# Optimization experiments

Measured on AMD Instinct MI355X. Metric: run time of the kernel, lower is better.

Reference implementation:

```python
import jax, jax.numpy as jnp
import numpy as np

D_MODEL = 2048
N_HEADS = 16
HEAD_DIM = D_MODEL // N_HEADS
SCALE = HEAD_DIM ** -0.5
LN_EPS = 1e-5
N_LAYERS = 24


def _layernorm(x, g, b):
    mu = jnp.mean(x, axis=-1, keepdims=True)
    var = jnp.mean(jnp.square(x - mu), axis=-1, keepdims=True)
    return (x - mu) * jax.lax.rsqrt(var + LN_EPS) * g + b


def _split_heads(x):  # [B,S,D] -> [B,H,S,hd]
    B, S, _ = x.shape
    return x.reshape(B, S, N_HEADS, HEAD_DIM).transpose(0, 2, 1, 3)


def setup_inputs() -> dict:
    key = jax.random.key(0)
    ks = jax.random.split(key, 12)
    B, St, Si = 2, 2048, 1024
    std_qkv = D_MODEL ** -0.5
    std_o = (2 * N_LAYERS) ** -0.5
    return {
        "q_text": jax.random.normal(ks[0], (B, St, D_MODEL), jnp.float32),
        "q_image": jax.random.normal(ks[1], (B, Si, D_MODEL), jnp.float32),
        "k_text": jax.random.normal(ks[2], (B, St, D_MODEL), jnp.float32),
        "k_image": jax.random.normal(ks[3], (B, Si, D_MODEL), jnp.float32),
        "Wq": jax.random.normal(ks[4], (D_MODEL, D_MODEL), jnp.float32) * std_qkv,
        "Wk": jax.random.normal(ks[5], (D_MODEL, D_MODEL), jnp.float32) * std_qkv,
        "Wv": jax.random.normal(ks[6], (D_MODEL, D_MODEL), jnp.float32) * std_qkv,
        "Wo": jax.random.normal(ks[7], (D_MODEL, D_MODEL), jnp.float32) * std_o,
        "ln_text_g": jnp.ones((D_MODEL,), jnp.float32),
        "ln_text_b": jnp.zeros((D_MODEL,), jnp.float32),
        "ln_image_g": jnp.ones((D_MODEL,), jnp.float32),
        "ln_image_b": jnp.zeros((D_MODEL,), jnp.float32),
    }


def reference(q_text, q_image, k_text, k_image, Wq, Wk, Wv, Wo,
              ln_text_g, ln_text_b, ln_image_g, ln_image_b):
    # Normalize each key modality once, project to K/V, concat along seq.
    kt = _layernorm(k_text, ln_text_g, ln_text_b)
    ki = _layernorm(k_image, ln_image_g, ln_image_b)
    concat_k = jnp.concatenate([_split_heads(kt @ Wk.T), _split_heads(ki @ Wk.T)], axis=2)
    concat_v = jnp.concatenate([_split_heads(kt @ Wv.T), _split_heads(ki @ Wv.T)], axis=2)

    def attend(q, g, b):
        B, S, _ = q.shape
        qn = _layernorm(q, g, b)
        qh = _split_heads(qn @ Wq.T) * SCALE            # [B,H,Sq,hd]
        scores = jnp.einsum('bhqd,bhkd->bhqk', qh, concat_k)
        attn = jax.nn.softmax(scores.astype(jnp.float32), axis=-1).astype(q.dtype)
        out = jnp.einsum('bhqk,bhkd->bhqd', attn, concat_v)
        out = out.transpose(0, 2, 1, 3).reshape(B, S, D_MODEL)
        return out @ Wo.T

    out_text = attend(q_text, ln_text_g, ln_text_b)
    out_image = attend(q_image, ln_image_g, ln_image_b)
    return (out_text, out_image)
```

## Files before the change

### kernel.cpp

```cpp
#include <hip/hip_runtime.h>

typedef __attribute__((ext_vector_type(8))) short bf16x8;
typedef __attribute__((ext_vector_type(4))) float f32x4;
typedef __attribute__((ext_vector_type(8))) unsigned short u16x8;

#define D_MODEL 2048
#define NH 16
#define HD 128
#define SKV 3072
#define QK_SCALE 0.08838834764831845f
#define LOG2E 1.4426950408889634f
#define DEFER_THR 11.5413f

__device__ __forceinline__ unsigned short f2bf(float f) {
  unsigned int u = __float_as_uint(f);
  u += 0x7fffu + ((u >> 16) & 1u);
  return (unsigned short)(u >> 16);
}
__device__ __forceinline__ float exp2hw(float x) {
  float r; asm("v_exp_f32 %0, %1" : "=v"(r) : "v"(x)); return r;
}
__device__ __forceinline__ unsigned int cvtpk(float lo, float hi) {
  unsigned int r; asm("v_cvt_pk_bf16_f32 %0, %1, %2" : "=v"(r) : "v"(lo), "v"(hi)); return r;
}

typedef __attribute__((address_space(1))) void as1_void;
typedef __attribute__((address_space(3))) void as3_void;
__device__ __forceinline__ void gload_lds16(const void* g, void* l) {
  __builtin_amdgcn_global_load_lds((as1_void*)g, (as3_void*)l, 16, 0, 0);
}

#define MFMA16(a, b, c) __builtin_amdgcn_mfma_f32_16x16x32_bf16((a), (b), (c), 0, 0, 0)

__global__ __launch_bounds__(256) void cvt_w_kernel(
    const float* __restrict__ s0, const float* __restrict__ s1,
    const float* __restrict__ s2, const float* __restrict__ s3,
    unsigned short* __restrict__ dstbase) {
  const int y = blockIdx.y;
  const float* src = (y == 0) ? s0 : (y == 1) ? s1 : (y == 2) ? s2 : s3;
  const float scale = (y == 0) ? (QK_SCALE * LOG2E) : 1.0f;
  unsigned short* dst = dstbase + (size_t)y * 4194304;
  int i = blockIdx.x * 256 + threadIdx.x;
  const float4* s = (const float4*)src + (size_t)i * 2;
  float4 a = s[0], b = s[1];
  u16x8 r;
  r[0] = f2bf(a.x * scale); r[1] = f2bf(a.y * scale);
  r[2] = f2bf(a.z * scale); r[3] = f2bf(a.w * scale);
  r[4] = f2bf(b.x * scale); r[5] = f2bf(b.y * scale);
  r[6] = f2bf(b.z * scale); r[7] = f2bf(b.w * scale);
  *((u16x8*)dst + i) = r;
}

__global__ __launch_bounds__(256) void ln_kernel(
    const float* __restrict__ x, const float* __restrict__ gw,
    const float* __restrict__ bw, unsigned short* __restrict__ out,
    int spb, int orpb, int obase) {
  const int row = blockIdx.x;
  const int t = threadIdx.x;
  const int b = row / spb, s = row - b * spb;
  const float* xr = x + (size_t)row * D_MODEL;
  unsigned short* orow = out + ((size_t)b * orpb + obase + s) * D_MODEL;

  float4 v0 = *(const float4*)(xr + t * 8);
  float4 v1 = *(const float4*)(xr + t * 8 + 4);
  float sum = v0.x + v0.y + v0.z + v0.w + v1.x + v1.y + v1.z + v1.w;
  float sq  = v0.x*v0.x + v0.y*v0.y + v0.z*v0.z + v0.w*v0.w
            + v1.x*v1.x + v1.y*v1.y + v1.z*v1.z + v1.w*v1.w;
#pragma unroll
  for (int o = 32; o > 0; o >>= 1) {
    sum += __shfl_down(sum, o);
    sq  += __shfl_down(sq, o);
  }
  __shared__ float red[8];
  const int wv = t >> 6, l = t & 63;
  if (l == 0) { red[wv] = sum; red[4 + wv] = sq; }
  __syncthreads();
  sum = red[0] + red[1] + red[2] + red[3];
  sq  = red[4] + red[5] + red[6] + red[7];
  const float mu = sum * (1.0f / 2048.0f);
  const float var = sq * (1.0f / 2048.0f) - mu * mu;
  const float rs = rsqrtf(var + 1e-5f);

  float4 g0 = *(const float4*)(gw + t * 8);
  float4 g1 = *(const float4*)(gw + t * 8 + 4);
  float4 b0 = *(const float4*)(bw + t * 8);
  float4 b1 = *(const float4*)(bw + t * 8 + 4);
  u16x8 r;
  r[0] = f2bf((v0.x - mu) * rs * g0.x + b0.x);
  r[1] = f2bf((v0.y - mu) * rs * g0.y + b0.y);
  r[2] = f2bf((v0.z - mu) * rs * g0.z + b0.z);
  r[3] = f2bf((v0.w - mu) * rs * g0.w + b0.w);
  r[4] = f2bf((v1.x - mu) * rs * g1.x + b1.x);
  r[5] = f2bf((v1.y - mu) * rs * g1.y + b1.y);
  r[6] = f2bf((v1.z - mu) * rs * g1.z + b1.z);
  r[7] = f2bf((v1.w - mu) * rs * g1.w + b1.w);
  *(u16x8*)(orow + t * 8) = r;
}

__global__ __launch_bounds__(256, 2) void gemm256x_kernel(
    const unsigned short* __restrict__ Aq, const unsigned short* __restrict__ Akv,
    const unsigned short* __restrict__ Wq, const unsigned short* __restrict__ Wk,
    const unsigned short* __restrict__ Wv,
    void* __restrict__ d0, void* __restrict__ d1,
    void* __restrict__ d2, void* __restrict__ d3, int mode) {
  __shared__ unsigned short lds3[3][12288];

  const int tid = threadIdx.x;
  const int wid = tid >> 6, l = tid & 63;
  const int wm = wid >> 1, wn = wid & 1;
  const int fr = l & 15, fg = l >> 4;
  const int rc = (fg * 8) ^ ((fr & 3) << 3);

  const int cpx = gridDim.x >> 3;
  int wg = ((int)blockIdx.x & 7) * cpx + ((int)blockIdx.x >> 3);

  const unsigned short* A = Aq;
  const unsigned short* W = Wq;
  int emode = mode;
  if (mode == 10) {
    int mat = wg / 384; wg -= mat * 384;
    if (mat == 0)      { emode = 0; }
    else if (mat == 1) { emode = 3; A = Akv; W = Wk; }
    else               { emode = 1; A = Akv; W = Wv; }
  }
  const int bm = wg >> 4, bn = wg & 15;

  const int lr = l >> 2;
  const int gsw = ((l & 3) ^ (lr & 3)) * 8;
  const unsigned short* gaBase = A + (size_t)(bm * 256 + wid * 64 + lr) * 2048 + gsw;
  const unsigned short* gbBase = W + (size_t)(bn * 128 + wid * 32 + lr) * 2048 + gsw;

#define STAGE(buf, kt) do {                                          \
    unsigned short* _da = &lds3[(buf)][wid * 2048];                  \
    unsigned short* _db = &lds3[(buf)][8192 + wid * 1024];           \
    const unsigned short* _sa = gaBase + (size_t)(kt) * 32;          \
    const unsigned short* _sb = gbBase + (size_t)(kt) * 32;          \
    gload_lds16(_sa,             _da);                               \
    gload_lds16(_sa + 16 * 2048, _da + 512);                         \
    gload_lds16(_sa + 32 * 2048, _da + 1024);                        \
    gload_lds16(_sa + 48 * 2048, _da + 1536);                        \
    gload_lds16(_sb,             _db);                               \
    gload_lds16(_sb + 16 * 2048, _db + 512);                         \
  } while (0)

  f32x4 acc[8][4] = {};
  bf16x8 af[8], bf01[2], bf23[2];

  STAGE(0, 0);
  STAGE(1, 1);
  asm volatile("s_waitcnt vmcnt(6)" ::: "memory");
  __builtin_amdgcn_s_barrier();
#pragma unroll
  for (int mi = 0; mi < 8; ++mi)
    af[mi] = *(const bf16x8*)&lds3[0][(wm * 128 + mi * 16 + fr) * 32 + rc];
#pragma unroll
  for (int ni = 0; ni < 2; ++ni)
    bf01[ni] = *(const bf16x8*)&lds3[0][8192 + (wn * 64 + ni * 16 + fr) * 32 + rc];

  int cur = 0;
  for (int t = 0; t < 64; ++t) {
#pragma unroll
    for (int ni = 0; ni < 2; ++ni)
      bf23[ni] = *(const bf16x8*)&lds3[cur][8192 + (wn * 64 + (ni + 2) * 16 + fr) * 32 + rc];
    if (t < 62) {
      int stg = cur + 2; if (stg >= 3) stg -= 3;
      STAGE(stg, t + 2);
    }

    __builtin_amdgcn_s_setprio(1);
#pragma unroll
    for (int mi = 0; mi < 8; ++mi)
#pragma unroll
      for (int ni = 0; ni < 2; ++ni)
        acc[mi][ni] = MFMA16(af[mi], bf01[ni], acc[mi][ni]);
    __builtin_amdgcn_s_setprio(0);

    __builtin_amdgcn_s_setprio(1);
#pragma unroll
    for (int mi = 0; mi < 8; ++mi)
#pragma unroll
      for (int ni = 0; ni < 2; ++ni)
        acc[mi][ni + 2] = MFMA16(af[mi], bf23[ni], acc[mi][ni + 2]);
    __builtin_amdgcn_s_setprio(0);

    __builtin_amdgcn_sched_barrier(0);
    if (t < 62) {
      asm volatile("s_waitcnt vmcnt(6)" ::: "memory");
      __builtin_amdgcn_s_barrier();
    } else if (t == 62) {
      asm volatile("s_waitcnt vmcnt(0)" ::: "memory");
      __builtin_amdgcn_s_barrier();
    }

    int nxt = cur + 1; if (nxt >= 3) nxt -= 3;
    if (t < 63) {
#pragma unroll
      for (int mi = 0; mi < 8; ++mi)
        af[mi] = *(const bf16x8*)&lds3[nxt][(wm * 128 + mi * 16 + fr) * 32 + rc];
#pragma unroll
      for (int ni = 0; ni < 2; ++ni)
        bf01[ni] = *(const bf16x8*)&lds3[nxt][8192 + (wn * 64 + ni * 16 + fr) * 32 + rc];
    }
    cur = nxt;
  }
#undef STAGE

#pragma unroll
  for (int mi = 0; mi < 8; ++mi) {
    const int row0 = bm * 256 + wm * 128 + mi * 16 + fg * 4;
    if (emode == 1) {
      int b = row0 / 3072, s0 = row0 - b * 3072;
#pragma unroll
      for (int ni = 0; ni < 4; ++ni) {
        int col = bn * 128 + wn * 64 + ni * 16 + fr;
        int hh = col >> 7, d = col & 127;
        size_t bh = (size_t)(b * NH + hh);
        size_t idx = (bh * 128 + d) * (size_t)3072 + ((s0 & ~31) | ((s0 & 31) ^ ((d & 3) << 3)));
        uint2 pk;
        pk.x = cvtpk(acc[mi][ni][0], acc[mi][ni][1]);
        pk.y = cvtpk(acc[mi][ni][2], acc[mi][ni][3]);
        *(uint2*)((unsigned short*)d3 + idx) = pk;
      }
    } else {
#pragma unroll
      for (int r = 0; r < 4; ++r) {
        int row = row0 + r;
#pragma unroll
        for (int ni = 0; ni < 4; ++ni) {
          int col = bn * 128 + wn * 64 + ni * 16 + fr;
          float v = acc[mi][ni][r];
          if (emode == 2) {
            ((float*)d0)[(size_t)row * 2048 + col] = v;
          } else if (emode == 0) {
            int hh = col >> 7, d = col & 127;
            if (row < 4096) {
              int b = row >> 11, s = row & 2047;
              ((unsigned short*)d0)[((size_t)(b * NH + hh) * 2048 + s) * 128 + d] = f2bf(v);
            } else {
              int rr = row - 4096, b = rr >> 10, s = rr & 1023;
              ((unsigned short*)d1)[((size_t)(b * NH + hh) * 1024 + s) * 128 + d] = f2bf(v);
            }
          } else {
            int b = row / 3072, s = row - b * 3072;
            int hh = col >> 7, d = col & 127;
            size_t bh = (size_t)(b * NH + hh);
            ((unsigned short*)d2)[(bh * 3072 + s) * 128 + (d ^ ((s & 7) << 3))] = f2bf(v);
          }
        }
      }
    }
  }
}

__global__ __launch_bounds__(256, 3) void attn_kernel(
    const unsigned short* __restrict__ Qt, const unsigned short* __restrict__ Qi,
    const unsigned short* __restrict__ Kh, const unsigned short* __restrict__ Vt,
    unsigned short* __restrict__ AOt, unsigned short* __restrict__ AOi) {
  __shared__ unsigned short Sh[20480];

  const int lin = blockIdx.x;
  const int w768 = (lin & 7) * 96 + (lin >> 3);
  const int qt24 = w768 % 24;
  const int hb   = w768 / 24;
  const int h = hb & 15, b = hb >> 4;
  const bool is_text = qt24 < 16;
  const int qt = is_text ? qt24 : qt24 - 16;
  const int Sq = is_text ? 2048 : 1024;
  const unsigned short* Qh = is_text ? Qt : Qi;
  unsigned short* AO = is_text ? AOt : AOi;

  const int tid = threadIdx.x;
  const int w = tid >> 6, l = tid & 63;
  const int fr = l & 15, fg = l >> 4;
  const size_t bh = (size_t)(b * NH + h);
  unsigned short* Pw = Sh + 16384 + w * 1024;

  const unsigned short* Qbase = Qh + (bh * Sq + (size_t)qt * 128 + w * 32) * HD;
  bf16x8 qf[2][4];
#pragma unroll
  for (int h2 = 0; h2 < 2; ++h2)
#pragma unroll
    for (int c = 0; c < 4; ++c)
      qf[h2][c] = *(const bf16x8*)(Qbase + (h2 * 16 + fr) * HD + c * 32 + fg * 8);

  f32x4 o[2][8] = {};
  float m[2]    = {-1e30f, -1e30f};
  float lsum[2] = {0.f, 0.f};

  const unsigned short* Kb = Kh + bh * (size_t)SKV * HD;
  const unsigned short* Vb = Vt + bh * (size_t)HD * SKV;

  const int swk = (fr & 7) << 3;
  const int swv = (fr & 3) << 3;

#define STAGE_K(kt, half) do {                                                   \
    unsigned short* _d = Sh + (half) * 4096 + w * 1024;                          \
    const unsigned short* _s = Kb + (size_t)((kt) * 32 + w * 8 + (l >> 4)) * 128 \
                               + (l & 15) * 8;                                   \
    gload_lds16(_s, _d);                                                         \
    gload_lds16(_s + 4 * 128, _d + 512);                                         \
  } while (0)
#define STAGE_V(kt, half) do {                                                   \
    unsigned short* _d = Sh + 8192 + (half) * 4096 + w * 1024;                   \
    const unsigned short* _s = Vb + (size_t)(w * 32 + (l >> 2)) * SKV            \
                               + (kt) * 32 + (l & 3) * 8;                        \
    gload_lds16(_s, _d);                                                         \
    gload_lds16(_s + 16 * SKV, _d + 512);                                        \
  } while (0)

  STAGE_K(0, 0);
  for (int kt = 0; kt < 96; ++kt) {
    const int half = kt & 1;
    STAGE_V(kt, half);
    asm volatile("s_waitcnt vmcnt(2)" ::: "memory");
    __builtin_amdgcn_s_barrier();

    const unsigned short* Ksc = Sh + half * 4096;
    f32x4 sT[2][2] = {};
#pragma unroll
    for (int j = 0; j < 2; ++j) {
      const int krb = (j * 16 + fr) * 128;
#pragma unroll
      for (int c = 0; c < 4; ++c) {
        bf16x8 kf = *(const bf16x8*)&Ksc[krb + ((c * 32 + fg * 8) ^ swk)];
        sT[0][j] = MFMA16(kf, qf[0][c], sT[0][j]);
        sT[1][j] = MFMA16(kf, qf[1][c], sT[1][j]);
      }
    }
    if (kt < 95) STAGE_K(kt + 1, half ^ 1);

#pragma unroll
    for (int h2 = 0; h2 < 2; ++h2) {
      float tm = fmaxf(fmaxf(fmaxf(sT[h2][0][0], sT[h2][0][1]),
                             fmaxf(sT[h2][0][2], sT[h2][0][3])),
                       fmaxf(fmaxf(sT[h2][1][0], sT[h2][1][1]),
                             fmaxf(sT[h2][1][2], sT[h2][1][3])));
      tm = fmaxf(tm, __shfl_xor(tm, 16));
      tm = fmaxf(tm, __shfl_xor(tm, 32));
      if (__any(tm - m[h2] > DEFER_THR)) {
        float mn = fmaxf(m[h2], tm);
        float al = exp2hw(m[h2] - mn);
#pragma unroll
        for (int nt = 0; nt < 8; ++nt) {
          f32x4 t = o[h2][nt];
          t[0] *= al; t[1] *= al; t[2] *= al; t[3] *= al;
          o[h2][nt] = t;
        }
        lsum[h2] *= al;
        m[h2] = mn;
      }
      const float mm = m[h2];
      float p00 = exp2hw(sT[h2][0][0] - mm), p01 = exp2hw(sT[h2][0][1] - mm);
      float p02 = exp2hw(sT[h2][0][2] - mm), p03 = exp2hw(sT[h2][0][3] - mm);
      float p10 = exp2hw(sT[h2][1][0] - mm), p11 = exp2hw(sT[h2][1][1] - mm);
      float p12 = exp2hw(sT[h2][1][2] - mm), p13 = exp2hw(sT[h2][1][3] - mm);
      lsum[h2] += (p00 + p01 + p02 + p03) + (p10 + p11 + p12 + p13);
      unsigned short* prow = &Pw[(h2 * 16 + fr) * 32];
      uint2 w0; w0.x = cvtpk(p00, p01); w0.y = cvtpk(p02, p03);
      uint2 w1; w1.x = cvtpk(p10, p11); w1.y = cvtpk(p12, p13);
      *(uint2*)(prow + ((fg * 4) ^ swv))      = w0;
      *(uint2*)(prow + ((16 + fg * 4) ^ swv)) = w1;
    }

    if (kt < 95) asm volatile("s_waitcnt vmcnt(2)" ::: "memory");
    else         asm volatile("s_waitcnt vmcnt(0)" ::: "memory");
    __builtin_amdgcn_s_barrier();

    asm volatile("s_waitcnt lgkmcnt(0)" ::: "memory");
    __builtin_amdgcn_sched_barrier(0);

    const unsigned short* Vsc = Sh + 8192 + half * 4096;
    bf16x8 pb[2];
#pragma unroll
    for (int h2 = 0; h2 < 2; ++h2)
      pb[h2] = *(const bf16x8*)&Pw[(h2 * 16 + fr) * 32 + ((fg * 8) ^ swv)];
#pragma unroll
    for (int nt = 0; nt < 8; ++nt) {
      bf16x8 vf = *(const bf16x8*)&Vsc[(nt * 16 + fr) * 32 + ((fg * 8) ^ swv)];
      o[0][nt] = MFMA16(vf, pb[0], o[0][nt]);
      o[1][nt] = MFMA16(vf, pb[1], o[1][nt]);
    }
    __builtin_amdgcn_s_barrier();
  }
#undef STAGE_K
#undef STAGE_V

  float inv[2];
#pragma unroll
  for (int h2 = 0; h2 < 2; ++h2) {
    float t = lsum[h2];
    t += __shfl_xor(t, 16);
    t += __shfl_xor(t, 32);
    inv[h2] = 1.0f / t;
  }
  unsigned short* Os = &Sh[w * 4096];
#pragma unroll
  for (int h2 = 0; h2 < 2; ++h2) {
    unsigned short* orow = &Os[(h2 * 16 + fr) * 128];
    const int sw8 = (fr & 7) << 3;
#pragma unroll
    for (int nt = 0; nt < 8; ++nt) {
      uint2 pk;
      pk.x = cvtpk(o[h2][nt][0] * inv[h2], o[h2][nt][1] * inv[h2]);
      pk.y = cvtpk(o[h2][nt][2] * inv[h2], o[h2][nt][3] * inv[h2]);
      *(uint2*)(orow + ((nt * 16 + fg * 4) ^ sw8)) = pk;
    }
  }
  asm volatile("s_waitcnt lgkmcnt(0)" ::: "memory");
  __builtin_amdgcn_sched_barrier(0);
  const int qr4 = l >> 4;
  const int dc = (l & 15) * 8;
  unsigned short* AObase = AO + ((size_t)b * Sq + (size_t)qt * 128 + w * 32) * D_MODEL + h * HD;
#pragma unroll
  for (int g = 0; g < 8; ++g) {
    const int row = g * 4 + qr4;
    bf16x8 v = *reinterpret_cast<const bf16x8*>(&Os[row * 128 + (dc ^ ((row & 7) << 3))]);
    *reinterpret_cast<bf16x8*>(&AObase[(size_t)row * D_MODEL + dc]) = v;
  }
}

extern "C" void kernel_launch(void* const* d_in, const int* in_sizes, int n_in,
                              void* d_out, int out_size, void* d_ws, size_t ws_size,
                              hipStream_t stream) {
  const float* q_text  = (const float*)d_in[0];
  const float* q_image = (const float*)d_in[1];
  const float* k_text  = (const float*)d_in[2];
  const float* k_image = (const float*)d_in[3];
  const float* Wq = (const float*)d_in[4];
  const float* Wk = (const float*)d_in[5];
  const float* Wv = (const float*)d_in[6];
  const float* Wo = (const float*)d_in[7];
  const float* ln_tg = (const float*)d_in[8];
  const float* ln_tb = (const float*)d_in[9];
  const float* ln_ig = (const float*)d_in[10];
  const float* ln_ib = (const float*)d_in[11];

  unsigned short* wq  = (unsigned short*)d_ws;
  unsigned short* wk  = wq  + 4194304;
  unsigned short* wv  = wk  + 4194304;
  unsigned short* wo  = wv  + 4194304;
  unsigned short* xqt = wo  + 4194304;
  unsigned short* xqi = xqt + 8388608;
  unsigned short* xk  = xqi + 4194304;
  unsigned short* qht = xk  + 12582912;
  unsigned short* qhi = qht + 8388608;
  unsigned short* kh  = qhi + 4194304;
  unsigned short* vt  = kh  + 12582912;
  const size_t needed = (size_t)(vt + 12582912 - wq) * 2;
  if (ws_size < needed) return;

  cvt_w_kernel<<<dim3(2048, 4), 256, 0, stream>>>(Wq, Wk, Wv, Wo, wq);

  ln_kernel<<<4096, 256, 0, stream>>>(q_text,  ln_tg, ln_tb, xqt, 2048, 2048, 0);
  ln_kernel<<<2048, 256, 0, stream>>>(q_image, ln_ig, ln_ib, xqi, 1024, 1024, 0);
  ln_kernel<<<4096, 256, 0, stream>>>(k_text,  ln_tg, ln_tb, xk, 2048, 3072, 0);
  ln_kernel<<<2048, 256, 0, stream>>>(k_image, ln_ig, ln_ib, xk, 1024, 3072, 2048);

  gemm256x_kernel<<<1152, 256, 0, stream>>>(xqt, xk, wq, wk, wv, qht, qhi, kh, vt, 10);

  attn_kernel<<<768, 256, 0, stream>>>(qht, qhi, kh, vt, xqt, xqi);

  gemm256x_kernel<<<384, 256, 0, stream>>>(xqt, nullptr, wo, nullptr, nullptr,
                                           d_out, nullptr, nullptr, nullptr, 2);
}
```

Baseline: 503.0 us.

## Double attention KV tile to 64, retune V swizzle, fuse layernorm launches

The attention kernel now processes 64 keys per iteration instead of 32. This doubles the K/V LDS tiles and the P buffer, and halves the number of loop iterations and barriers. The V transpose swizzle in the QKV GEMM epilogue changes to a 64-wide pattern with an (d&7) XOR so it matches the new LDS layout, and MFMA sections get s_setprio hints. The four layernorm launches are merged into one kernel. The cost is doubled shared memory in attention and occupancy lowered from 3 to 2 blocks per CU.

Result: no change. 504.8 us (+0.4%).

```diff
diff --git a/kernel.cpp b/kernel.cpp
--- a/kernel.cpp
+++ b/kernel.cpp
@@ -51,18 +51,25 @@
   *((u16x8*)dst + i) = r;
 }
 
-__global__ __launch_bounds__(256) void ln_kernel(
-    const float* __restrict__ x, const float* __restrict__ gw,
-    const float* __restrict__ bw, unsigned short* __restrict__ out,
-    int spb, int orpb, int obase) {
-  const int row = blockIdx.x;
+__global__ __launch_bounds__(256) void ln_all_kernel(
+    const float* __restrict__ qt, const float* __restrict__ qi,
+    const float* __restrict__ ktx, const float* __restrict__ kix,
+    const float* __restrict__ gt, const float* __restrict__ bt,
+    const float* __restrict__ gi, const float* __restrict__ bi,
+    unsigned short* __restrict__ xqt, unsigned short* __restrict__ xqi,
+    unsigned short* __restrict__ xk) {
+  const int rid = blockIdx.x;
   const int t = threadIdx.x;
-  const int b = row / spb, s = row - b * spb;
-  const float* xr = x + (size_t)row * D_MODEL;
-  unsigned short* orow = out + ((size_t)b * orpb + obase + s) * D_MODEL;
-
-  float4 v0 = *(const float4*)(xr + t * 8);
-  float4 v1 = *(const float4*)(xr + t * 8 + 4);
+  const float* src; const float* gw; const float* bw; unsigned short* dst;
+  if (rid < 4096)      { src = qt + (size_t)rid * 2048; gw = gt; bw = bt; dst = xqt + (size_t)rid * 2048; }
+  else if (rid < 6144) { int r = rid - 4096; src = qi + (size_t)r * 2048; gw = gi; bw = bi; dst = xqi + (size_t)r * 2048; }
+  else if (rid < 10240){ int r = rid - 6144; src = ktx + (size_t)r * 2048; gw = gt; bw = bt;
+                         int b = r >> 11, s = r & 2047; dst = xk + ((size_t)b * 3072 + s) * 2048; }
+  else                 { int r = rid - 10240; src = kix + (size_t)r * 2048; gw = gi; bw = bi;
+                         int b = r >> 10, s = r & 1023; dst = xk + ((size_t)b * 3072 + 2048 + s) * 2048; }
+
+  float4 v0 = *(const float4*)(src + t * 8);
+  float4 v1 = *(const float4*)(src + t * 8 + 4);
   float sum = v0.x + v0.y + v0.z + v0.w + v1.x + v1.y + v1.z + v1.w;
   float sq  = v0.x*v0.x + v0.y*v0.y + v0.z*v0.z + v0.w*v0.w
             + v1.x*v1.x + v1.y*v1.y + v1.z*v1.z + v1.w*v1.w;
@@ -94,7 +101,7 @@
   r[5] = f2bf((v1.y - mu) * rs * g1.y + b1.y);
   r[6] = f2bf((v1.z - mu) * rs * g1.z + b1.z);
   r[7] = f2bf((v1.w - mu) * rs * g1.w + b1.w);
-  *(u16x8*)(orow + t * 8) = r;
+  *(u16x8*)(dst + t * 8) = r;
 }
 
 __global__ __launch_bounds__(256, 2) void gemm256x_kernel(
@@ -215,7 +222,8 @@
         int col = bn * 128 + wn * 64 + ni * 16 + fr;
         int hh = col >> 7, d = col & 127;
         size_t bh = (size_t)(b * NH + hh);
-        size_t idx = (bh * 128 + d) * (size_t)3072 + ((s0 & ~31) | ((s0 & 31) ^ ((d & 3) << 3)));
+        size_t idx = (bh * 128 + d) * (size_t)3072
+                   + ((s0 & ~63) | ((s0 & 63) ^ ((d & 7) << 3)));
         uint2 pk;
         pk.x = cvtpk(acc[mi][ni][0], acc[mi][ni][1]);
         pk.y = cvtpk(acc[mi][ni][2], acc[mi][ni][3]);
@@ -252,11 +260,11 @@
   }
 }
 
-__global__ __launch_bounds__(256, 3) void attn_kernel(
+__global__ __launch_bounds__(256, 2) void attn_kernel(
     const unsigned short* __restrict__ Qt, const unsigned short* __restrict__ Qi,
     const unsigned short* __restrict__ Kh, const unsigned short* __restrict__ Vt,
     unsigned short* __restrict__ AOt, unsigned short* __restrict__ AOi) {
-  __shared__ unsigned short Sh[20480];
+  __shared__ unsigned short Sh[40960];
 
   const int lin = blockIdx.x;
   const int w768 = (lin & 7) * 96 + (lin >> 3);
@@ -273,7 +281,7 @@
   const int w = tid >> 6, l = tid & 63;
   const int fr = l & 15, fg = l >> 4;
   const size_t bh = (size_t)(b * NH + h);
-  unsigned short* Pw = Sh + 16384 + w * 1024;
+  unsigned short* Pw = Sh + 32768 + w * 2048;
 
   const unsigned short* Qbase = Qh + (bh * Sq + (size_t)qt * 128 + w * 32) * HD;
   bf16x8 qf[2][4];
@@ -291,34 +299,38 @@
   const unsigned short* Vb = Vt + bh * (size_t)HD * SKV;
 
   const int swk = (fr & 7) << 3;
-  const int swv = (fr & 3) << 3;
 
 #define STAGE_K(kt, half) do {                                                   \
-    unsigned short* _d = Sh + (half) * 4096 + w * 1024;                          \
-    const unsigned short* _s = Kb + (size_t)((kt) * 32 + w * 8 + (l >> 4)) * 128 \
+    unsigned short* _d = Sh + (half) * 8192 + w * 2048;                          \
+    const unsigned short* _s = Kb + (size_t)((kt) * 64 + w * 16 + (l >> 4)) * 128\
                                + (l & 15) * 8;                                   \
-    gload_lds16(_s, _d);                                                         \
-    gload_lds16(_s + 4 * 128, _d + 512);                                         \
+    gload_lds16(_s,            _d);                                              \
+    gload_lds16(_s + 4 * 128,  _d + 512);                                        \
+    gload_lds16(_s + 8 * 128,  _d + 1024);                                       \
+    gload_lds16(_s + 12 * 128, _d + 1536);                                       \
   } while (0)
 #define STAGE_V(kt, half) do {                                                   \
-    unsigned short* _d = Sh + 8192 + (half) * 4096 + w * 1024;                   \
-    const unsigned short* _s = Vb + (size_t)(w * 32 + (l >> 2)) * SKV            \
-                               + (kt) * 32 + (l & 3) * 8;                        \
-    gload_lds16(_s, _d);                                                         \
-    gload_lds16(_s + 16 * SKV, _d + 512);                                        \
+    unsigned short* _d = Sh + 16384 + (half) * 8192 + w * 2048;                  \
+    const unsigned short* _s = Vb + (size_t)(w * 32 + (l >> 3)) * SKV            \
+                               + (kt) * 64 + (l & 7) * 8;                        \
+    gload_lds16(_s,             _d);                                             \
+    gload_lds16(_s + 8 * SKV,   _d + 512);                                       \
+    gload_lds16(_s + 16 * SKV,  _d + 1024);                                      \
+    gload_lds16(_s + 24 * SKV,  _d + 1536);                                      \
   } while (0)
 
   STAGE_K(0, 0);
-  for (int kt = 0; kt < 96; ++kt) {
+  for (int kt = 0; kt < SKV / 64; ++kt) {
     const int half = kt & 1;
     STAGE_V(kt, half);
-    asm volatile("s_waitcnt vmcnt(2)" ::: "memory");
+    asm volatile("s_waitcnt vmcnt(4)" ::: "memory");
     __builtin_amdgcn_s_barrier();
 
-    const unsigned short* Ksc = Sh + half * 4096;
-    f32x4 sT[2][2] = {};
-#pragma unroll
-    for (int j = 0; j < 2; ++j) {
+    const unsigned short* Ksc = Sh + half * 8192;
+    f32x4 sT[2][4] = {};
+    __builtin_amdgcn_s_setprio(1);
+#pragma unroll
+    for (int j = 0; j < 4; ++j) {
       const int krb = (j * 16 + fr) * 128;
 #pragma unroll
       for (int c = 0; c < 4; ++c) {
@@ -327,14 +339,16 @@
         sT[1][j] = MFMA16(kf, qf[1][c], sT[1][j]);
       }
     }
-    if (kt < 95) STAGE_K(kt + 1, half ^ 1);
+    __builtin_amdgcn_s_setprio(0);
+    if (kt < 47) STAGE_K(kt + 1, half ^ 1);
 
 #pragma unroll
     for (int h2 = 0; h2 < 2; ++h2) {
-      float tm = fmaxf(fmaxf(fmaxf(sT[h2][0][0], sT[h2][0][1]),
-                             fmaxf(sT[h2][0][2], sT[h2][0][3])),
-                       fmaxf(fmaxf(sT[h2][1][0], sT[h2][1][1]),
-                             fmaxf(sT[h2][1][2], sT[h2][1][3])));
+      float tm = sT[h2][0][0];
+#pragma unroll
+      for (int j = 0; j < 4; ++j)
+#pragma unroll
+        for (int r = 0; r < 4; ++r) tm = fmaxf(tm, sT[h2][j][r]);
       tm = fmaxf(tm, __shfl_xor(tm, 16));
       tm = fmaxf(tm, __shfl_xor(tm, 32));
       if (__any(tm - m[h2] > DEFER_THR)) {
@@ -350,36 +364,47 @@
         m[h2] = mn;
       }
       const float mm = m[h2];
-      float p00 = exp2hw(sT[h2][0][0] - mm), p01 = exp2hw(sT[h2][0][1] - mm);
-      float p02 = exp2hw(sT[h2][0][2] - mm), p03 = exp2hw(sT[h2][0][3] - mm);
-      float p10 = exp2hw(sT[h2][1][0] - mm), p11 = exp2hw(sT[h2][1][1] - mm);
-      float p12 = exp2hw(sT[h2][1][2] - mm), p13 = exp2hw(sT[h2][1][3] - mm);
-      lsum[h2] += (p00 + p01 + p02 + p03) + (p10 + p11 + p12 + p13);
-      unsigned short* prow = &Pw[(h2 * 16 + fr) * 32];
-      uint2 w0; w0.x = cvtpk(p00, p01); w0.y = cvtpk(p02, p03);
-      uint2 w1; w1.x = cvtpk(p10, p11); w1.y = cvtpk(p12, p13);
-      *(uint2*)(prow + ((fg * 4) ^ swv))      = w0;
-      *(uint2*)(prow + ((16 + fg * 4) ^ swv)) = w1;
-    }
-
-    if (kt < 95) asm volatile("s_waitcnt vmcnt(2)" ::: "memory");
+      float ps = 0.f;
+      unsigned short* prow = &Pw[(h2 * 16 + fr) * 64];
+#pragma unroll
+      for (int j = 0; j < 4; ++j) {
+        float p0 = exp2hw(sT[h2][j][0] - mm);
+        float p1 = exp2hw(sT[h2][j][1] - mm);
+        float p2 = exp2hw(sT[h2][j][2] - mm);
+        float p3 = exp2hw(sT[h2][j][3] - mm);
+        ps += (p0 + p1) + (p2 + p3);
+        uint2 pk; pk.x = cvtpk(p0, p1); pk.y = cvtpk(p2, p3);
+        *(uint2*)(prow + ((j * 16 + fg * 4) ^ swk)) = pk;
+      }
+      lsum[h2] += ps;
+    }
+
+    if (kt < 47) asm volatile("s_waitcnt vmcnt(4)" ::: "memory");
     else         asm volatile("s_waitcnt vmcnt(0)" ::: "memory");
     __builtin_amdgcn_s_barrier();
 
     asm volatile("s_waitcnt lgkmcnt(0)" ::: "memory");
     __builtin_amdgcn_sched_barrier(0);
 
-    const unsigned short* Vsc = Sh + 8192 + half * 4096;
-    bf16x8 pb[2];
+    const unsigned short* Vsc = Sh + 16384 + half * 8192;
+    bf16x8 pb[2][2];
 #pragma unroll
     for (int h2 = 0; h2 < 2; ++h2)
-      pb[h2] = *(const bf16x8*)&Pw[(h2 * 16 + fr) * 32 + ((fg * 8) ^ swv)];
+#pragma unroll
+      for (int kc = 0; kc < 2; ++kc)
+        pb[h2][kc] = *(const bf16x8*)&Pw[(h2 * 16 + fr) * 64 + ((kc * 32 + fg * 8) ^ swk)];
+    __builtin_amdgcn_s_setprio(1);
 #pragma unroll
     for (int nt = 0; nt < 8; ++nt) {
-      bf16x8 vf = *(const bf16x8*)&Vsc[(nt * 16 + fr) * 32 + ((fg * 8) ^ swv)];
-      o[0][nt] = MFMA16(vf, pb[0], o[0][nt]);
-      o[1][nt] = MFMA16(vf, pb[1], o[1][nt]);
-    }
+      const int vrb = (nt * 16 + fr) * 64;
+#pragma unroll
+      for (int kc = 0; kc < 2; ++kc) {
+        bf16x8 vf = *(const bf16x8*)&Vsc[vrb + ((kc * 32 + fg * 8) ^ swk)];
+        o[0][nt] = MFMA16(vf, pb[0][kc], o[0][nt]);
+        o[1][nt] = MFMA16(vf, pb[1][kc], o[1][nt]);
+      }
+    }
+    __builtin_amdgcn_s_setprio(0);
     __builtin_amdgcn_s_barrier();
   }
 #undef STAGE_K
@@ -451,10 +476,9 @@
 
   cvt_w_kernel<<<dim3(2048, 4), 256, 0, stream>>>(Wq, Wk, Wv, Wo, wq);
 
-  ln_kernel<<<4096, 256, 0, stream>>>(q_text,  ln_tg, ln_tb, xqt, 2048, 2048, 0);
-  ln_kernel<<<2048, 256, 0, stream>>>(q_image, ln_ig, ln_ib, xqi, 1024, 1024, 0);
-  ln_kernel<<<4096, 256, 0, stream>>>(k_text,  ln_tg, ln_tb, xk, 2048, 3072, 0);
-  ln_kernel<<<2048, 256, 0, stream>>>(k_image, ln_ig, ln_ib, xk, 1024, 3072, 2048);
+  ln_all_kernel<<<12288, 256, 0, stream>>>(q_text, q_image, k_text, k_image,
+                                           ln_tg, ln_tb, ln_ig, ln_ib,
+                                           xqt, xqi, xk);
 
   gemm256x_kernel<<<1152, 256, 0, stream>>>(xqt, xk, wq, wk, wv, qht, qhi, kh, vt, 10);
 
```
